# Kernel tuning notes

Hardware: AMD Instinct MI355X
Metric: run time of the kernel (lower is better)

Reference implementation:

```python
import jax, jax.numpy as jnp
import numpy as np

ALPHA = 8.3  # depth-similarity decay from Depth-aware CNN
K = 3        # kernel size
PAD = 1      # padding (stride=1, dilation=1)


def _patches(x, k, pad):
    """Extract kxk stride-1 patches. x: (B,C,H,W) -> (B,C,k,k,H,W)."""
    B, C, H, W = x.shape
    xp = jnp.pad(x, ((0, 0), (0, 0), (pad, pad), (pad, pad)))
    rows = []
    for i in range(k):
        cols = [xp[:, :, i:i + H, j:j + W] for j in range(k)]
        rows.append(jnp.stack(cols, axis=2))          # (B,C,k,H,W)
    return jnp.stack(rows, axis=2)                     # (B,C,k,k,H,W)


def setup_inputs() -> dict:
    key = jax.random.key(0)
    k1, k2, k3 = jax.random.split(key, 3)
    B, Cin, H, W = 8, 512, 64, 64
    Cout = 64
    x = jax.random.normal(k1, (B, Cin, H, W), dtype=jnp.float32)
    depth = jax.random.uniform(k2, (B, 1, H, W), dtype=jnp.float32)
    stdv = 1.0 / np.sqrt(Cin * K * K)
    weight = jax.random.uniform(k3, (Cout, Cin, K, K), dtype=jnp.float32,
                                minval=-stdv, maxval=stdv)
    return {"input": x, "depth": depth, "weight": weight}


def reference(input, depth, weight):
    # depth-modulated conv: out(p0) = sum_pn w(pn) * x(p0+pn) * exp(-a*|d(p0)-d(p0+pn)|)
    xpat = _patches(input, K, PAD)                 # (B,Cin,K,K,H,W)
    dpat = _patches(depth, K, PAD)                 # (B,1,K,K,H,W)
    d0 = depth[:, :, None, None, :, :]             # center depth (B,1,1,1,H,W)
    gate = jnp.exp(-ALPHA * jnp.abs(d0 - dpat))    # (B,1,K,K,H,W)
    out = jnp.einsum('ocij,bcijhw->bohw', weight, xpat * gate)
    return out
```

## Files before the change

### kernel.cpp

```cpp
#include <hip/hip_runtime.h>
#include <math.h>

#define ALPHA 8.3f
#define STAGE_BYTES 26112

typedef short v8s  __attribute__((ext_vector_type(8)));
typedef float v16f __attribute__((ext_vector_type(16)));
typedef float v4f  __attribute__((ext_vector_type(4)));

static __device__ __forceinline__ unsigned short f2bf(float f) {
    unsigned int u = __float_as_uint(f);
    u = (u + 0x7fffu + ((u >> 16) & 1u)) >> 16;
    return (unsigned short)u;
}

static __device__ __forceinline__ void async16(const void* g, void* l) {
    __builtin_amdgcn_global_load_lds(
        (const __attribute__((address_space(1))) unsigned int*)g,
        (__attribute__((address_space(3))) unsigned int*)l, 16, 0, 0);
}

__global__ void prep_weights(const float* __restrict__ w, unsigned short* __restrict__ wt,
                             float* __restrict__ zb) {
    if (blockIdx.x == 0) zb[threadIdx.x] = 0.f;
    int i = blockIdx.x * 256 + threadIdx.x;
    if (i >= 9 * 32 * 2 * 64 * 8) return;
    int j    = i & 7;
    int lane = (i >> 3) & 63;
    int mt   = (i >> 9) & 1;
    int ks   = (i >> 10) & 31;
    int tap  = i >> 15;
    int o = mt * 32 + (lane & 31);
    int c = ks * 16 + (lane >> 5) * 8 + j;
    wt[i] = f2bf(w[(o * 512 + c) * 9 + tap]);
}

__global__ __launch_bounds__(256) void nhwc_cast(const float* __restrict__ x,
                                                 unsigned short* __restrict__ x2) {
    __shared__ float st[64][65];
    const int bx  = blockIdx.x;
    const int ch2 = bx & 1;
    const int h   = (bx >> 1) & 63;
    const int b   = bx >> 7;
    const int tid = threadIdx.x;
    const float* xb = x + ((size_t)b * 512 + ch2 * 256) * 4096 + h * 64;
    unsigned short* ob = x2 + (((size_t)b * 64 + h) * 64) * 512 + ch2 * 256;
    for (int cb = 0; cb < 4; ++cb) {
        __syncthreads();
#pragma unroll
        for (int i = 0; i < 4; ++i) {
            const int c  = i * 16 + (tid >> 4);
            const int w4 = (tid & 15) * 4;
            const float4 v = *(const float4*)&xb[(size_t)(cb * 64 + c) * 4096 + w4];
            st[c][w4]     = v.x;
            st[c][w4 + 1] = v.y;
            st[c][w4 + 2] = v.z;
            st[c][w4 + 3] = v.w;
        }
        __syncthreads();
#pragma unroll
        for (int j = 0; j < 2; ++j) {
            const int idx = j * 256 + tid;
            const int w = idx >> 3, k = idx & 7;
            unsigned short t[8];
#pragma unroll
            for (int e = 0; e < 8; ++e) t[e] = f2bf(st[k * 8 + e][w]);
            uint4 u;
            u.x = t[0] | ((unsigned)t[1] << 16);
            u.y = t[2] | ((unsigned)t[3] << 16);
            u.z = t[4] | ((unsigned)t[5] << 16);
            u.w = t[6] | ((unsigned)t[7] << 16);
            *(uint4*)&ob[(size_t)w * 512 + cb * 64 + k * 8] = u;
        }
    }
}

__global__ __launch_bounds__(1024, 4)
void depthconv_v6(const unsigned short* __restrict__ x2,
                  const float* __restrict__ depth,
                  const unsigned short* __restrict__ wt,
                  const float* __restrict__ zbuf,
                  float* __restrict__ out) {
    __shared__ __align__(16) char smem[2 * STAGE_BYTES];

    const int bx   = blockIdx.x;
    const int xcd  = bx & 7;
    const int i0   = bx >> 3;
    const int wt2  = i0 & 1;
    const int b    = (i0 >> 1) & 7;
    const int ht   = xcd * 2 + (i0 >> 4);
    const int h0 = ht * 4, w0 = wt2 * 32;

    const int tid  = threadIdx.x;
    const int wid  = tid >> 6;
    const int lane = tid & 63;
    const int l31  = lane & 31;
    const int half = lane >> 5;
    const int mt   = wid & 1;
    const int rt   = (wid >> 1) & 3;
    const int kh   = wid >> 3;

    const char* xpix = (const char*)(x2 + ((size_t)b * 4096) * 512);

    float gt[9];
    {
        const float* dp = depth + (size_t)b * 4096;
        const int hq = h0 + rt, wq = w0 + l31;
        const float d0 = dp[hq * 64 + wq];
#pragma unroll
        for (int t = 0; t < 9; ++t) {
            const int hn = hq + t / 3 - 1, wn = wq + t % 3 - 1;
            const float dn = (hn >= 0 && hn < 64 && wn >= 0 && wn < 64) ? dp[hn * 64 + wn] : 0.f;
            gt[t] = __expf(-ALPHA * fabsf(d0 - dn));
        }
    }

    v16f acc;
    v16f vzero;
#pragma unroll
    for (int r = 0; r < 16; ++r) { acc[r] = 0.f; vzero[r] = 0.f; }

#define ISSUE(SS)                                                               \
    {                                                                           \
        const int ss_ = (SS);                                                   \
        char* bufb = smem + (ss_ & 1) * STAGE_BYTES;                            \
        _Pragma("unroll")                                                       \
        for (int it = 0; it < 2; ++it) {                                        \
            const int i = it * 1024 + tid;                                      \
            if (i < 1632) {                                                     \
                const int slice = i >> 3;                                       \
                const int gg = (i & 7) ^ (slice & 7);                           \
                const int r = slice / 34;                                       \
                const int c = slice - r * 34;                                   \
                const int hh = h0 - 1 + r, ww = w0 - 1 + c;                     \
                const char* gp = (hh >= 0 && hh < 64 && ww >= 0 && ww < 64)     \
                    ? xpix + (size_t)(hh * 64 + ww) * 1024                      \
                           + (gg >> 2) * 512 + ss_ * 64 + (gg & 3) * 16        \
                    : (const char*)zbuf;                                        \
                async16(gp, bufb + (size_t)i * 16);                             \
            }                                                                   \
        }                                                                       \
    }

    ISSUE(0);

    const int g0 = kh * 4 + half;
    const int g1 = g0 + 2;

    for (int ss = 0; ss < 8; ++ss) {
        __syncthreads();
        if (ss < 7) ISSUE(ss + 1);
        const char* bufb = smem + (ss & 1) * STAGE_BYTES;
        const int ks0 = kh * 16 + ss * 2;
#pragma unroll
        for (int tap = 0; tap < 9; ++tap) {
            const int di = tap / 3, dj = tap % 3;
            const v8s a0 = *(const v8s*)&wt[(((tap * 32 + ks0) * 2 + mt) * 64 + lane) * 8];
            const v8s a1 = *(const v8s*)&wt[(((tap * 32 + ks0 + 1) * 2 + mt) * 64 + lane) * 8];
            const int slice = (rt + di) * 34 + l31 + dj;
            const int s7 = slice & 7;
            const v8s b0 = *(const v8s*)(bufb + ((size_t)(slice * 8 + (g0 ^ s7))) * 16);
            const v8s b1 = *(const v8s*)(bufb + ((size_t)(slice * 8 + (g1 ^ s7))) * 16);
            v16f pass = __builtin_amdgcn_mfma_f32_32x32x16_bf16(a0, b0, vzero, 0, 0, 0);
            pass = __builtin_amdgcn_mfma_f32_32x32x16_bf16(a1, b1, pass, 0, 0, 0);
            const float gv = gt[tap];
#pragma unroll
            for (int r = 0; r < 16; ++r)
                acc[r] = fmaf(gv, pass[r], acc[r]);
        }
    }

    __syncthreads();
    float* red = (float*)smem;
    const int region = mt * 4 + rt;
    if (kh == 1) {
#pragma unroll
        for (int qd = 0; qd < 4; ++qd) {
            v4f v;
            v[0] = acc[qd * 4];     v[1] = acc[qd * 4 + 1];
            v[2] = acc[qd * 4 + 2]; v[3] = acc[qd * 4 + 3];
            *(v4f*)&red[region * 1024 + lane * 16 + qd * 4] = v;
        }
    }
    __syncthreads();
    if (kh == 0) {
        float* ob = out + ((size_t)b * 64) * 4096 + (h0 + rt) * 64 + w0;
#pragma unroll
        for (int qd = 0; qd < 4; ++qd) {
            const v4f v = *(const v4f*)&red[region * 1024 + lane * 16 + qd * 4];
#pragma unroll
            for (int j = 0; j < 4; ++j) {
                const int rg = qd * 4 + j;
                const int o = mt * 32 + (rg & 3) + 8 * (rg >> 2) + 4 * half;
                ob[(size_t)o * 4096 + l31] = acc[rg] + v[j];
            }
        }
    }
}

extern "C" void kernel_launch(void* const* d_in, const int* in_sizes, int n_in,
                              void* d_out, int out_size, void* d_ws, size_t ws_size,
                              hipStream_t stream) {
    const float* x      = (const float*)d_in[0];
    const float* depth  = (const float*)d_in[1];
    const float* weight = (const float*)d_in[2];
    float* out = (float*)d_out;

    unsigned short* wtb = (unsigned short*)d_ws;
    float* zbuf         = (float*)((char*)d_ws + 786432);
    unsigned short* x2  = (unsigned short*)((char*)d_ws + (1 << 20));

    prep_weights<<<1152, 256, 0, stream>>>(weight, wtb, zbuf);
    nhwc_cast<<<1024, 256, 0, stream>>>(x, x2);
    depthconv_v6<<<256, 1024, 0, stream>>>(x2, depth, wtb, zbuf, out);
}
```

Baseline: 144.4 us.

## Restructure depth conv to accumulate per-column taps and apply gate after MFMA

The main conv kernel now gives each workgroup one output row and six waves, split by output-channel half and kernel row. Each wave keeps three MFMA accumulators, one per kernel column, and applies the depth gates once after the channel loop instead of doing a gated FMA after every tap. Stages now cover 128 channels, so there are 4 pipeline stages instead of 8. The weight layout and NHWC cast grid are reshaped to match, and the cast uses more, smaller blocks. This removes the per-tap VALU scaling and the cross-wave K split, at the cost of more accumulator registers and a 3-way LDS reduction.

Result: slower. 157.5 us (+9.0%).

```diff
diff --git a/kernel.cpp b/kernel.cpp
--- a/kernel.cpp
+++ b/kernel.cpp
@@ -24,63 +24,64 @@
                              float* __restrict__ zb) {
     if (blockIdx.x == 0) zb[threadIdx.x] = 0.f;
     int i = blockIdx.x * 256 + threadIdx.x;
-    if (i >= 9 * 32 * 2 * 64 * 8) return;
-    int j    = i & 7;
-    int lane = (i >> 3) & 63;
-    int mt   = (i >> 9) & 1;
-    int ks   = (i >> 10) & 31;
-    int tap  = i >> 15;
-    int o = mt * 32 + (lane & 31);
-    int c = ks * 16 + (lane >> 5) * 8 + j;
-    wt[i] = f2bf(w[(o * 512 + c) * 9 + tap]);
+    if (i >= 294912) return;
+    int j     = i & 7;
+    int lane  = (i >> 3) & 63;
+    int F     = i >> 9;
+    int chunk = F & 7;
+    int t     = F >> 3;
+    int tap   = t % 9;
+    int sm    = t / 9;
+    int mt    = sm & 1;
+    int ss    = sm >> 1;
+    int o   = mt * 32 + (lane & 31);
+    int cin = ss * 128 + chunk * 16 + (lane >> 5) * 8 + j;
+    wt[i] = f2bf(w[(o * 512 + cin) * 9 + tap]);
 }
 
 __global__ __launch_bounds__(256) void nhwc_cast(const float* __restrict__ x,
                                                  unsigned short* __restrict__ x2) {
     __shared__ float st[64][65];
-    const int bx  = blockIdx.x;
-    const int ch2 = bx & 1;
-    const int h   = (bx >> 1) & 63;
-    const int b   = bx >> 7;
+    const int bx = blockIdx.x;
+    const int cq = bx & 7;
+    const int h  = (bx >> 3) & 63;
+    const int b  = bx >> 9;
     const int tid = threadIdx.x;
-    const float* xb = x + ((size_t)b * 512 + ch2 * 256) * 4096 + h * 64;
-    unsigned short* ob = x2 + (((size_t)b * 64 + h) * 64) * 512 + ch2 * 256;
-    for (int cb = 0; cb < 4; ++cb) {
-        __syncthreads();
-#pragma unroll
-        for (int i = 0; i < 4; ++i) {
-            const int c  = i * 16 + (tid >> 4);
-            const int w4 = (tid & 15) * 4;
-            const float4 v = *(const float4*)&xb[(size_t)(cb * 64 + c) * 4096 + w4];
-            st[c][w4]     = v.x;
-            st[c][w4 + 1] = v.y;
-            st[c][w4 + 2] = v.z;
-            st[c][w4 + 3] = v.w;
-        }
-        __syncthreads();
-#pragma unroll
-        for (int j = 0; j < 2; ++j) {
-            const int idx = j * 256 + tid;
-            const int w = idx >> 3, k = idx & 7;
-            unsigned short t[8];
-#pragma unroll
-            for (int e = 0; e < 8; ++e) t[e] = f2bf(st[k * 8 + e][w]);
-            uint4 u;
-            u.x = t[0] | ((unsigned)t[1] << 16);
-            u.y = t[2] | ((unsigned)t[3] << 16);
-            u.z = t[4] | ((unsigned)t[5] << 16);
-            u.w = t[6] | ((unsigned)t[7] << 16);
-            *(uint4*)&ob[(size_t)w * 512 + cb * 64 + k * 8] = u;
-        }
-    }
-}
-
-__global__ __launch_bounds__(1024, 4)
-void depthconv_v6(const unsigned short* __restrict__ x2,
-                  const float* __restrict__ depth,
-                  const unsigned short* __restrict__ wt,
-                  const float* __restrict__ zbuf,
-                  float* __restrict__ out) {
+    const float* xb = x + ((size_t)b * 512 + cq * 64) * 4096 + h * 64;
+    unsigned short* ob = x2 + (((size_t)b * 64 + h) * 64) * 512 + cq * 64;
+#pragma unroll
+    for (int i = 0; i < 4; ++i) {
+        const int c  = i * 16 + (tid >> 4);
+        const int w4 = (tid & 15) * 4;
+        const float4 v = *(const float4*)&xb[(size_t)c * 4096 + w4];
+        st[c][w4]     = v.x;
+        st[c][w4 + 1] = v.y;
+        st[c][w4 + 2] = v.z;
+        st[c][w4 + 3] = v.w;
+    }
+    __syncthreads();
+#pragma unroll
+    for (int j = 0; j < 2; ++j) {
+        const int idx = j * 256 + tid;
+        const int w = idx >> 3, k = idx & 7;
+        unsigned short t[8];
+#pragma unroll
+        for (int e = 0; e < 8; ++e) t[e] = f2bf(st[k * 8 + e][w]);
+        uint4 u;
+        u.x = t[0] | ((unsigned)t[1] << 16);
+        u.y = t[2] | ((unsigned)t[3] << 16);
+        u.z = t[4] | ((unsigned)t[5] << 16);
+        u.w = t[6] | ((unsigned)t[7] << 16);
+        *(uint4*)&ob[(size_t)w * 512 + k * 8] = u;
+    }
+}
+
+__global__ __launch_bounds__(384, 3)
+void depthconv_v10(const unsigned short* __restrict__ x2,
+                   const float* __restrict__ depth,
+                   const unsigned short* __restrict__ wt,
+                   const float* __restrict__ zbuf,
+                   float* __restrict__ out) {
     __shared__ __align__(16) char smem[2 * STAGE_BYTES];
 
     const int bx   = blockIdx.x;
@@ -88,8 +89,8 @@
     const int i0   = bx >> 3;
     const int wt2  = i0 & 1;
     const int b    = (i0 >> 1) & 7;
-    const int ht   = xcd * 2 + (i0 >> 4);
-    const int h0 = ht * 4, w0 = wt2 * 32;
+    const int h0   = xcd * 8 + (i0 >> 4);
+    const int w0   = wt2 * 32;
 
     const int tid  = threadIdx.x;
     const int wid  = tid >> 6;
@@ -97,45 +98,44 @@
     const int l31  = lane & 31;
     const int half = lane >> 5;
     const int mt   = wid & 1;
-    const int rt   = (wid >> 1) & 3;
-    const int kh   = wid >> 3;
+    const int di   = wid >> 1;
 
     const char* xpix = (const char*)(x2 + ((size_t)b * 4096) * 512);
 
-    float gt[9];
+    float gt[3];
     {
         const float* dp = depth + (size_t)b * 4096;
-        const int hq = h0 + rt, wq = w0 + l31;
-        const float d0 = dp[hq * 64 + wq];
-#pragma unroll
-        for (int t = 0; t < 9; ++t) {
-            const int hn = hq + t / 3 - 1, wn = wq + t % 3 - 1;
+        const float d0 = dp[h0 * 64 + w0 + l31];
+        const int hn = h0 + di - 1;
+#pragma unroll
+        for (int dj = 0; dj < 3; ++dj) {
+            const int wn = w0 + l31 + dj - 1;
             const float dn = (hn >= 0 && hn < 64 && wn >= 0 && wn < 64) ? dp[hn * 64 + wn] : 0.f;
-            gt[t] = __expf(-ALPHA * fabsf(d0 - dn));
-        }
-    }
-
-    v16f acc;
-    v16f vzero;
-#pragma unroll
-    for (int r = 0; r < 16; ++r) { acc[r] = 0.f; vzero[r] = 0.f; }
+            gt[dj] = __expf(-ALPHA * fabsf(d0 - dn));
+        }
+    }
+
+    v16f acc[3];
+#pragma unroll
+    for (int d = 0; d < 3; ++d)
+#pragma unroll
+        for (int r = 0; r < 16; ++r) acc[d][r] = 0.f;
 
 #define ISSUE(SS)                                                               \
     {                                                                           \
         const int ss_ = (SS);                                                   \
         char* bufb = smem + (ss_ & 1) * STAGE_BYTES;                            \
         _Pragma("unroll")                                                       \
-        for (int it = 0; it < 2; ++it) {                                        \
-            const int i = it * 1024 + tid;                                      \
+        for (int it = 0; it < 5; ++it) {                                        \
+            const int i = it * 384 + tid;                                       \
             if (i < 1632) {                                                     \
-                const int slice = i >> 3;                                       \
-                const int gg = (i & 7) ^ (slice & 7);                           \
+                const int slice = i >> 4;                                       \
+                const int g = (i & 15) ^ (slice & 7);                           \
                 const int r = slice / 34;                                       \
                 const int c = slice - r * 34;                                   \
                 const int hh = h0 - 1 + r, ww = w0 - 1 + c;                     \
                 const char* gp = (hh >= 0 && hh < 64 && ww >= 0 && ww < 64)     \
-                    ? xpix + (size_t)(hh * 64 + ww) * 1024                      \
-                           + (gg >> 2) * 512 + ss_ * 64 + (gg & 3) * 16        \
+                    ? xpix + (size_t)(hh * 64 + ww) * 1024 + ss_ * 256 + g * 16 \
                     : (const char*)zbuf;                                        \
                 async16(gp, bufb + (size_t)i * 16);                             \
             }                                                                   \
@@ -144,55 +144,58 @@
 
     ISSUE(0);
 
-    const int g0 = kh * 4 + half;
-    const int g1 = g0 + 2;
-
-    for (int ss = 0; ss < 8; ++ss) {
+    for (int ss = 0; ss < 4; ++ss) {
         __syncthreads();
-        if (ss < 7) ISSUE(ss + 1);
+        if (ss < 3) ISSUE(ss + 1);
         const char* bufb = smem + (ss & 1) * STAGE_BYTES;
-        const int ks0 = kh * 16 + ss * 2;
-#pragma unroll
-        for (int tap = 0; tap < 9; ++tap) {
-            const int di = tap / 3, dj = tap % 3;
-            const v8s a0 = *(const v8s*)&wt[(((tap * 32 + ks0) * 2 + mt) * 64 + lane) * 8];
-            const v8s a1 = *(const v8s*)&wt[(((tap * 32 + ks0 + 1) * 2 + mt) * 64 + lane) * 8];
-            const int slice = (rt + di) * 34 + l31 + dj;
+        const unsigned short* wp =
+            wt + (size_t)(((ss * 2 + mt) * 9 + di * 3) * 8) * 512 + (size_t)lane * 8;
+#pragma unroll
+        for (int dj = 0; dj < 3; ++dj) {
+            const int slice = di * 34 + l31 + dj;
             const int s7 = slice & 7;
-            const v8s b0 = *(const v8s*)(bufb + ((size_t)(slice * 8 + (g0 ^ s7))) * 16);
-            const v8s b1 = *(const v8s*)(bufb + ((size_t)(slice * 8 + (g1 ^ s7))) * 16);
-            v16f pass = __builtin_amdgcn_mfma_f32_32x32x16_bf16(a0, b0, vzero, 0, 0, 0);
-            pass = __builtin_amdgcn_mfma_f32_32x32x16_bf16(a1, b1, pass, 0, 0, 0);
-            const float gv = gt[tap];
-#pragma unroll
-            for (int r = 0; r < 16; ++r)
-                acc[r] = fmaf(gv, pass[r], acc[r]);
-        }
+#pragma unroll
+            for (int ch = 0; ch < 8; ++ch) {
+                const v8s a = *(const v8s*)(wp + (size_t)(dj * 8 + ch) * 512);
+                const int slot = (ch * 2 + half) ^ s7;
+                const v8s bb = *(const v8s*)(bufb + (size_t)(slice * 16 + slot) * 16);
+                acc[dj] = __builtin_amdgcn_mfma_f32_32x32x16_bf16(a, bb, acc[dj], 0, 0, 0);
+            }
+        }
+    }
+
+    float m[16];
+#pragma unroll
+    for (int r = 0; r < 16; ++r) {
+        m[r] = gt[0] * acc[0][r];
+        m[r] = fmaf(gt[1], acc[1][r], m[r]);
+        m[r] = fmaf(gt[2], acc[2][r], m[r]);
     }
 
     __syncthreads();
     float* red = (float*)smem;
-    const int region = mt * 4 + rt;
-    if (kh == 1) {
+    if (di > 0) {
+        const int region = mt * 2 + (di - 1);
 #pragma unroll
         for (int qd = 0; qd < 4; ++qd) {
             v4f v;
-            v[0] = acc[qd * 4];     v[1] = acc[qd * 4 + 1];
-            v[2] = acc[qd * 4 + 2]; v[3] = acc[qd * 4 + 3];
-            *(v4f*)&red[region * 1024 + lane * 16 + qd * 4] = v;
+            v[0] = m[qd * 4];     v[1] = m[qd * 4 + 1];
+            v[2] = m[qd * 4 + 2]; v[3] = m[qd * 4 + 3];
+            *(v4f*)&red[(size_t)region * 1024 + lane * 16 + qd * 4] = v;
         }
     }
     __syncthreads();
-    if (kh == 0) {
-        float* ob = out + ((size_t)b * 64) * 4096 + (h0 + rt) * 64 + w0;
+    if (di == 0) {
+        float* ob = out + ((size_t)b * 64) * 4096 + h0 * 64 + w0;
 #pragma unroll
         for (int qd = 0; qd < 4; ++qd) {
-            const v4f v = *(const v4f*)&red[region * 1024 + lane * 16 + qd * 4];
+            const v4f v1 = *(const v4f*)&red[(size_t)(mt * 2) * 1024 + lane * 16 + qd * 4];
+            const v4f v2 = *(const v4f*)&red[(size_t)(mt * 2 + 1) * 1024 + lane * 16 + qd * 4];
 #pragma unroll
             for (int j = 0; j < 4; ++j) {
                 const int rg = qd * 4 + j;
                 const int o = mt * 32 + (rg & 3) + 8 * (rg >> 2) + 4 * half;
-                ob[(size_t)o * 4096 + l31] = acc[rg] + v[j];
+                ob[(size_t)o * 4096 + l31] = m[rg] + v1[j] + v2[j];
             }
         }
     }
@@ -211,6 +214,6 @@
     unsigned short* x2  = (unsigned short*)((char*)d_ws + (1 << 20));
 
     prep_weights<<<1152, 256, 0, stream>>>(weight, wtb, zbuf);
-    nhwc_cast<<<1024, 256, 0, stream>>>(x, x2);
-    depthconv_v6<<<256, 1024, 0, stream>>>(x2, depth, wtb, zbuf, out);
-}
+    nhwc_cast<<<4096, 256, 0, stream>>>(x, x2);
+    depthconv_v10<<<1024, 384, 0, stream>>>(x2, depth, wtb, zbuf, out);
+}
```
